# Kernel optimization log

Measured on AMD Instinct MI355X. Metric: run time of the kernel, lower is better.

Reference implementation:

```python
import jax, jax.numpy as jnp
import numpy as np

NUM_NODES = 100000
NUM_EDGES = 1600000
INPUT_DIM = 128
NUM_LAYERS = 3
EPS = 1e-12


def setup_inputs() -> dict:
    key = jax.random.key(0)
    k1, k2, k3, k4, k5 = jax.random.split(key, 5)
    emb = jax.random.normal(k1, (NUM_NODES, INPUT_DIM), dtype=jnp.float32)
    edge_index = jax.random.randint(k2, (2, NUM_EDGES), 0, NUM_NODES, dtype=jnp.int64)
    senders = jax.random.randint(k3, (16384,), 0, NUM_NODES, dtype=jnp.int64)
    receivers = jax.random.randint(k4, (16384,), 0, NUM_NODES, dtype=jnp.int64)
    mlp_dim = INPUT_DIM * (NUM_LAYERS + 1)  # concat aggregation -> 512
    W = jax.random.normal(k5, (mlp_dim, mlp_dim), dtype=jnp.float32) * 0.02
    b = jnp.zeros((mlp_dim,), dtype=jnp.float32)
    return {"emb": emb, "edge_index": edge_index, "senders": senders,
            "receivers": receivers, "W": W, "b": b}


def _l2_normalize(x):
    # matches F.normalize(x, p=2, dim=-1) with eps=1e-12
    n = jnp.linalg.norm(x, axis=-1, keepdims=True)
    return x / jnp.maximum(n, EPS)


def reference(emb, edge_index, senders, receivers, W, b):
    src, dst = edge_index[0], edge_index[1]
    # LightGCN-style symmetric degree normalization: 1/sqrt(d_src * d_dst)
    ones = jnp.ones((src.shape[0],), dtype=emb.dtype)
    deg = jax.ops.segment_sum(ones, dst, num_segments=NUM_NODES)
    deg = jnp.maximum(deg, 1.0)
    dinv = jax.lax.rsqrt(deg)
    norm = dinv[src] * dinv[dst]  # [E]

    x = emb
    z = [_l2_normalize(x)]
    for _ in range(NUM_LAYERS):
        msgs = x[src] * norm[:, None]                      # [E, D] gather + scale
        x = jax.ops.segment_sum(msgs, dst, num_segments=NUM_NODES)  # scatter-add
        z.append(_l2_normalize(x))
    x = jnp.concatenate(z, axis=-1)        # [N, D*(L+1)]
    x = x @ W.T + b                        # post_mlp
    return (x[senders], x[receivers])
```

## Files before the change

kernel.cpp:

```cpp
#include <hip/hip_runtime.h>

#define NN 100000
#define NE 1600000
#define DD 128
#define MD 512
#define SEL 16384
#define MROWS 32768
#define NBKT 196
#define TILE 4096
#define SEGCAP 16384
#define NBINA ((NE + TILE - 1) / TILE)
#define NMARK ((2 * SEL + 255) / 256)
#define NCOMP ((NN + 255) / 256)

typedef __attribute__((ext_vector_type(8))) short bf16x8;
typedef __attribute__((ext_vector_type(4))) float f32x4;

__device__ __forceinline__ unsigned short f2bf(float f) {
  unsigned u = __float_as_uint(f);
  u += 0x7fff + ((u >> 16) & 1);
  return (unsigned short)(u >> 16);
}
__device__ __forceinline__ float bflo(unsigned v) { return __uint_as_float(v << 16); }
__device__ __forceinline__ float bfhi(unsigned v) { return __uint_as_float(v & 0xffff0000u); }

__global__ __launch_bounds__(256) void k_binA_mark(const int* __restrict__ src,
                                                   const int* __restrict__ dst,
                                                   int* __restrict__ gcursor,
                                                   unsigned* __restrict__ ebuf,
                                                   const int* __restrict__ sl,
                                                   const int* __restrict__ rl,
                                                   int* __restrict__ mark) {
  if (blockIdx.x >= NBINA) {
    const int i = (blockIdx.x - NBINA) * 256 + threadIdx.x;
    if (i < SEL) mark[sl[i]] = 1;
    else if (i < 2 * SEL) mark[rl[i - SEL]] = 1;
    return;
  }
  __shared__ int hist[NBKT];
  __shared__ int base[NBKT];
  __shared__ int cnt2[NBKT];
  const int tid = threadIdx.x;
  const long e0 = (long)blockIdx.x * TILE;
  for (int i = tid; i < NBKT; i += 256) { hist[i] = 0; cnt2[i] = 0; }
  __syncthreads();
  unsigned pk[16]; int bk[16];
  #pragma unroll
  for (int k = 0; k < 16; ++k) {
    const long e = e0 + k * 256 + tid;
    bk[k] = -1;
    if (e < NE) {
      const int d = dst[e], s = src[e];
      bk[k] = d >> 9;
      pk[k] = ((unsigned)s << 9) | (unsigned)(d & 511);
      atomicAdd(&hist[bk[k]], 1);
    }
  }
  __syncthreads();
  for (int i = tid; i < NBKT; i += 256)
    base[i] = i * SEGCAP + atomicAdd(&gcursor[i], hist[i]);
  __syncthreads();
  #pragma unroll
  for (int k = 0; k < 16; ++k) {
    if (bk[k] >= 0) {
      const int lp = atomicAdd(&cnt2[bk[k]], 1);
      ebuf[base[bk[k]] + lp] = pk[k];
    }
  }
}

__global__ __launch_bounds__(256) void k_degB_compact(const unsigned* __restrict__ ebuf,
                                                      const int* __restrict__ bcnt,
                                                      int* __restrict__ deg,
                                                      float* __restrict__ dinv,
                                                      int* __restrict__ excl,
                                                      int* __restrict__ btot,
                                                      unsigned short* __restrict__ x0,
                                                      unsigned short* __restrict__ x1,
                                                      unsigned short* __restrict__ x2,
                                                      const int* __restrict__ mark,
                                                      int* __restrict__ list,
                                                      int* __restrict__ lcnt,
                                                      int* __restrict__ uidx) {
  if (blockIdx.x >= NBKT) {
    const int n = (blockIdx.x - NBKT) * 256 + threadIdx.x;
    if (n < NN && mark[n]) {
      const int p = atomicAdd(lcnt, 1);
      list[p] = n;
      uidx[n] = p;
    }
    return;
  }
  __shared__ int ld[512];
  __shared__ int ps[256];
  const int b = blockIdx.x;
  const int n0 = b << 9;
  const int nn = min(512, NN - n0);
  const int tid = threadIdx.x;
  for (int i = tid; i < 512; i += 256) ld[i] = 0;
  __syncthreads();
  const int s0 = b * SEGCAP;
  const int c = bcnt[b];
  for (int i = tid; i < c; i += 256) atomicAdd(&ld[ebuf[s0 + i] & 511], 1);
  __syncthreads();
  const int d0 = (tid * 2 < nn) ? ld[tid * 2] : 0;
  const int d1 = (tid * 2 + 1 < nn) ? ld[tid * 2 + 1] : 0;
  const int p0 = (d0 + 7) & ~7, p1 = (d1 + 7) & ~7;
  ps[tid] = p0 + p1;
  __syncthreads();
  for (int o = 1; o < 256; o <<= 1) {
    int t2 = (tid >= o) ? ps[tid - o] : 0;
    __syncthreads();
    ps[tid] += t2;
    __syncthreads();
  }
  const int exbase = ps[tid] - (p0 + p1);
  if (tid * 2 < nn) {
    deg[n0 + tid * 2] = d0;
    dinv[n0 + tid * 2] = rsqrtf(fmaxf((float)d0, 1.f));
    excl[n0 + tid * 2] = exbase;
  }
  if (tid * 2 + 1 < nn) {
    deg[n0 + tid * 2 + 1] = d1;
    dinv[n0 + tid * 2 + 1] = rsqrtf(fmaxf((float)d1, 1.f));
    excl[n0 + tid * 2 + 1] = exbase + p0;
  }
  if (tid == 255) btot[b] = ps[255];
  if (b == 0 && tid < 64) {
    ((unsigned*)(x0 + (size_t)NN * DD))[tid] = 0u;
    ((unsigned*)(x1 + (size_t)NN * DD))[tid] = 0u;
    ((unsigned*)(x2 + (size_t)NN * DD))[tid] = 0u;
  }
}

__global__ __launch_bounds__(256) void k_binB(const unsigned* __restrict__ ebuf,
                                              const int* __restrict__ bcnt,
                                              const int* __restrict__ btot,
                                              const int* __restrict__ excl,
                                              const int* __restrict__ degI,
                                              int2* __restrict__ nodeinfo,
                                              int* __restrict__ csr) {
  __shared__ int seg[SEGCAP];
  __shared__ int rs[512];
  __shared__ int cnt[512];
  __shared__ int sm[256];
  const int b = blockIdx.x;
  const int n0 = b << 9;
  const int nn = min(512, NN - n0);
  const int tid = threadIdx.x;
  int v = (tid < NBKT) ? btot[tid] : 0;
  sm[tid] = v;
  __syncthreads();
  for (int o = 1; o < 256; o <<= 1) {
    int t2 = (tid >= o) ? sm[tid - o] : 0;
    __syncthreads();
    sm[tid] += t2;
    __syncthreads();
  }
  const int seg0 = b ? sm[b - 1] : 0;
  const int seglen = btot[b];
  for (int i = tid; i < nn; i += 256) {
    const int ex = excl[n0 + i];
    rs[i] = ex;
    cnt[i] = 0;
    const int cp = (degI[n0 + i] + 7) & ~7;
    nodeinfo[n0 + i] = make_int2(seg0 + ex, cp);
  }
  for (int i = tid; i < seglen; i += 256) seg[i] = NN << 8;
  __syncthreads();
  const int s0 = b * SEGCAP;
  const int c = bcnt[b];
  for (int i = tid; i < c; i += 256) {
    const unsigned e = ebuf[s0 + i];
    const int dl = e & 511;
    const int pos = rs[dl] + atomicAdd(&cnt[dl], 1);
    seg[pos] = (int)((e >> 9) << 8);
  }
  __syncthreads();
  for (int i = tid; i < seglen; i += 256) csr[seg0 + i] = seg[i];
}

__global__ __launch_bounds__(256) void k_aggs(const int2* __restrict__ nodeinfo,
                                              const int* __restrict__ csr,
                                              const float* __restrict__ dinv,
                                              const unsigned short* __restrict__ xin,
                                              unsigned short* __restrict__ xout) {
  const int lane = threadIdx.x & 63;
  const int hi = lane >> 5, l5 = lane & 31;
  const int bid = blockIdx.x;
  const int xcd = bid & 7;
  const int h = xcd >> 2;
  const int g = (bid >> 3) * 4 + (xcd & 3);
  const int wvh = g * 4 + (threadIdx.x >> 6);
  const int stride = gridDim.x * 2;
  const char* xb = (const char*)xin;
  const unsigned lc = (unsigned)(h * 128 + l5 * 4);
  for (int p = wvh; 2 * p < NN; p += stride) {
    const int idx = 2 * p + hi;
    const bool act = idx < NN;
    const int n = act ? idx : 0;
    const int2 ni = nodeinfo[n];
    const int start = ni.x;
    const int cntp = act ? ni.y : 0;
    float ax[8], ay[8];
    #pragma unroll
    for (int u = 0; u < 8; ++u) { ax[u] = 0.f; ay[u] = 0.f; }
    for (int j = 0; j < cntp; j += 8) {
      const int4 e0 = *(const int4*)(csr + start + j);
      const int4 e1 = *(const int4*)(csr + start + j + 4);
      unsigned v[8];
      v[0] = *(const unsigned*)(xb + ((unsigned)e0.x + lc));
      v[1] = *(const unsigned*)(xb + ((unsigned)e0.y + lc));
      v[2] = *(const unsigned*)(xb + ((unsigned)e0.z + lc));
      v[3] = *(const unsigned*)(xb + ((unsigned)e0.w + lc));
      v[4] = *(const unsigned*)(xb + ((unsigned)e1.x + lc));
      v[5] = *(const unsigned*)(xb + ((unsigned)e1.y + lc));
      v[6] = *(const unsigned*)(xb + ((unsigned)e1.z + lc));
      v[7] = *(const unsigned*)(xb + ((unsigned)e1.w + lc));
      #pragma unroll
      for (int u = 0; u < 8; ++u) { ax[u] += bflo(v[u]); ay[u] += bfhi(v[u]); }
    }
    if (act) {
      const float s = dinv[n] * dinv[n];
      const float rx = (((ax[0] + ax[1]) + (ax[2] + ax[3])) + ((ax[4] + ax[5]) + (ax[6] + ax[7]))) * s;
      const float ry = (((ay[0] + ay[1]) + (ay[2] + ay[3])) + ((ay[4] + ay[5]) + (ay[6] + ay[7]))) * s;
      *(unsigned*)((char*)xout + ((unsigned)n << 8) + lc) =
          ((unsigned)f2bf(ry) << 16) | f2bf(rx);
    }
  }
}

__global__ __launch_bounds__(256) void k_agg3z(const int2* __restrict__ nodeinfo,
                                               const int* __restrict__ csr,
                                               const float* __restrict__ dinv,
                                               const unsigned short* __restrict__ x0,
                                               const unsigned short* __restrict__ x1,
                                               const unsigned short* __restrict__ x2,
                                               unsigned short* __restrict__ zbuf,
                                               const int* __restrict__ list,
                                               const int* __restrict__ lcnt) {
  const int lane = threadIdx.x & 63;
  const int wv = (blockIdx.x * blockDim.x + threadIdx.x) >> 6;
  const int nw = (gridDim.x * blockDim.x) >> 6;
  const int cl = *lcnt;
  const char* xb2 = (const char*)x2;
  const unsigned lc = (unsigned)(lane * 4);
  for (int r = wv; r < cl; r += nw) {
    const int n = list[r];
    const int2 ni = nodeinfo[n];
    const int start = ni.x;
    const int cntp = ni.y;
    float ax[8], ay[8];
    #pragma unroll
    for (int u = 0; u < 8; ++u) { ax[u] = 0.f; ay[u] = 0.f; }
    for (int j = 0; j < cntp; j += 8) {
      const int4 e0 = *(const int4*)(csr + start + j);
      const int4 e1 = *(const int4*)(csr + start + j + 4);
      unsigned v[8];
      v[0] = *(const unsigned*)(xb2 + ((unsigned)e0.x + lc));
      v[1] = *(const unsigned*)(xb2 + ((unsigned)e0.y + lc));
      v[2] = *(const unsigned*)(xb2 + ((unsigned)e0.z + lc));
      v[3] = *(const unsigned*)(xb2 + ((unsigned)e0.w + lc));
      v[4] = *(const unsigned*)(xb2 + ((unsigned)e1.x + lc));
      v[5] = *(const unsigned*)(xb2 + ((unsigned)e1.y + lc));
      v[6] = *(const unsigned*)(xb2 + ((unsigned)e1.z + lc));
      v[7] = *(const unsigned*)(xb2 + ((unsigned)e1.w + lc));
      #pragma unroll
      for (int u = 0; u < 8; ++u) { ax[u] += bflo(v[u]); ay[u] += bfhi(v[u]); }
    }
    const float s = dinv[n] * dinv[n];
    const float rx = (((ax[0] + ax[1]) + (ax[2] + ax[3])) + ((ax[4] + ax[5]) + (ax[6] + ax[7]))) * s;
    const float ry = (((ay[0] + ay[1]) + (ay[2] + ay[3])) + ((ay[4] + ay[5]) + (ay[6] + ay[7]))) * s;
    {
      float ss = fmaf(rx, rx, ry * ry);
      #pragma unroll
      for (int m = 32; m >= 1; m >>= 1) ss += __shfl_xor(ss, m);
      const float sc = 1.0f / fmaxf(sqrtf(ss), 1e-12f);
      *(unsigned*)(zbuf + (size_t)r * MD + 384 + lane * 2) =
          ((unsigned)f2bf(ry * sc) << 16) | f2bf(rx * sc);
    }
    unsigned v0 = *(const unsigned*)((const char*)x0 + ((unsigned)n << 8) + lc);
    unsigned v1 = *(const unsigned*)((const char*)x1 + ((unsigned)n << 8) + lc);
    unsigned v2 = *(const unsigned*)((const char*)x2 + ((unsigned)n << 8) + lc);
    unsigned vv[3] = {v0, v1, v2};
    #pragma unroll
    for (int q = 0; q < 3; ++q) {
      const float a = bflo(vv[q]), b = bfhi(vv[q]);
      float ss = fmaf(a, a, b * b);
      #pragma unroll
      for (int m = 32; m >= 1; m >>= 1) ss += __shfl_xor(ss, m);
      const float sc = 1.0f / fmaxf(sqrtf(ss), 1e-12f);
      *(unsigned*)(zbuf + (size_t)r * MD + q * DD + lane * 2) =
          ((unsigned)f2bf(b * sc) << 16) | f2bf(a * sc);
    }
  }
}

__global__ __launch_bounds__(256) void k_conv_emb2(const float* __restrict__ emb,
                                                   const float* __restrict__ dinv,
                                                   unsigned short* __restrict__ x0,
                                                   const float* __restrict__ W,
                                                   unsigned short* __restrict__ Wbf) {
  if (blockIdx.x >= NN / 4) {
    const int i = (blockIdx.x - NN / 4) * 256 + threadIdx.x;
    if (i < MD * MD / 4) {
      float4 v = ((const float4*)W)[i];
      ushort4 o;
      o.x = f2bf(v.x); o.y = f2bf(v.y); o.z = f2bf(v.z); o.w = f2bf(v.w);
      ((ushort4*)Wbf)[i] = o;
    }
    return;
  }
  const int lane = threadIdx.x & 63;
  const int n = blockIdx.x * 4 + (threadIdx.x >> 6);
  const float2 v = ((const float2*)(emb + (size_t)n * DD))[lane];
  const float d = dinv[n];
  *(unsigned*)(x0 + (size_t)n * DD + lane * 2) =
      ((unsigned)f2bf(v.y * d) << 16) | f2bf(v.x * d);
}

__global__ __launch_bounds__(256) void k_gemm(const unsigned short* __restrict__ zbuf,
                                              const int* __restrict__ sl,
                                              const int* __restrict__ rl,
                                              const int* __restrict__ uidx,
                                              const unsigned short* __restrict__ B,
                                              const float* __restrict__ bias,
                                              float* __restrict__ out) {
  __shared__ __align__(16) char smraw[20480];
  unsigned short (*As)[40] = (unsigned short(*)[40])smraw;
  unsigned short (*Bs)[40] = (unsigned short(*)[40])(smraw + 10240);
  float (*et)[132] = (float(*)[132])smraw;
  const int t = threadIdx.x;
  const int bid = blockIdx.x;
  const int xcd = bid & 7;
  const int j = bid >> 3;
  const int mt = xcd * 32 + (j >> 2);
  const int nt = j & 3;
  const int i0 = mt * 128, j0 = nt * 128;
  const int lane = t & 63, wid = t >> 6;
  const int wr = wid >> 1, wc = wid & 1;
  const int fr = lane & 15, kg = lane >> 4;
  const int srow = t >> 2, seg = t & 3;
  const int r0 = i0 + srow, r1 = r0 + 64;
  const int nd0 = (r0 < SEL) ? sl[r0] : rl[r0 - SEL];
  const int nd1 = (r1 < SEL) ? sl[r1] : rl[r1 - SEL];
  const unsigned short* pa0 = zbuf + (size_t)uidx[nd0] * MD + seg * 8;
  const unsigned short* pa1 = zbuf + (size_t)uidx[nd1] * MD + seg * 8;
  const unsigned short* pb0 = B + (size_t)(j0 + srow) * MD + seg * 8;
  const unsigned short* pb1 = B + (size_t)(j0 + srow + 64) * MD + seg * 8;
  f32x4 acc[4][4] = {};
  for (int k0 = 0; k0 < MD; k0 += 32) {
    *(float4*)(&As[srow][seg * 8]) = *(const float4*)(pa0 + k0);
    *(float4*)(&As[srow + 64][seg * 8]) = *(const float4*)(pa1 + k0);
    *(float4*)(&Bs[srow][seg * 8]) = *(const float4*)(pb0 + k0);
    *(float4*)(&Bs[srow + 64][seg * 8]) = *(const float4*)(pb1 + k0);
    __syncthreads();
    bf16x8 af[4], bfr[4];
    #pragma unroll
    for (int m = 0; m < 4; ++m)
      af[m] = *(const bf16x8*)(&As[wr * 64 + m * 16 + fr][kg * 8]);
    #pragma unroll
    for (int n = 0; n < 4; ++n)
      bfr[n] = *(const bf16x8*)(&Bs[wc * 64 + n * 16 + fr][kg * 8]);
    #pragma unroll
    for (int m = 0; m < 4; ++m)
      #pragma unroll
      for (int n = 0; n < 4; ++n)
        acc[m][n] = __builtin_amdgcn_mfma_f32_16x16x32_bf16(af[m], bfr[n], acc[m][n], 0, 0, 0);
    __syncthreads();
  }
  #pragma unroll
  for (int m = 0; m < 4; ++m) {
    __syncthreads();
    #pragma unroll
    for (int n = 0; n < 4; ++n)
      #pragma unroll
      for (int r = 0; r < 4; ++r)
        et[wr * 16 + kg * 4 + r][wc * 64 + n * 16 + fr] = acc[m][n][r];
    __syncthreads();
    #pragma unroll
    for (int w = 0; w < 4; ++w) {
      const int idx = w * 256 + t;
      const int lrow = idx >> 5, lc4 = idx & 31;
      const int grow = i0 + (lrow >> 4) * 64 + m * 16 + (lrow & 15);
      const int gcol = j0 + lc4 * 4;
      const float4 bv = *(const float4*)(bias + gcol);
      float4 o;
      o.x = et[lrow][lc4 * 4 + 0] + bv.x;
      o.y = et[lrow][lc4 * 4 + 1] + bv.y;
      o.z = et[lrow][lc4 * 4 + 2] + bv.z;
      o.w = et[lrow][lc4 * 4 + 3] + bv.w;
      *(float4*)(out + (size_t)grow * MD + gcol) = o;
    }
  }
}

extern "C" void kernel_launch(void* const* d_in, const int* in_sizes, int n_in,
                              void* d_out, int out_size, void* d_ws, size_t ws_size,
                              hipStream_t stream) {
  const float* emb = (const float*)d_in[0];
  const int* ei = (const int*)d_in[1];
  const int* esrc = ei;
  const int* edst = ei + NE;
  const int* send = (const int*)d_in[2];
  const int* recv = (const int*)d_in[3];
  const float* W = (const float*)d_in[4];
  const float* bias = (const float*)d_in[5];
  float* out = (float*)d_out;

  char* ws = (char*)d_ws;
  size_t off = 0;
  auto take = [&](size_t b) {
    char* p = ws + off;
    off = (off + b + 1023) & ~(size_t)1023;
    return p;
  };
  const size_t CSRN = (size_t)NE + 8 * (size_t)NN;
  int* zblk = (int*)take((size_t)(NBKT + 1 + NN) * 4);
  int* gcursor = zblk;
  int* lcnt = zblk + NBKT;
  int* mark = zblk + NBKT + 1;
  int* uidx = (int*)take((size_t)NN * 4);
  float* dinv = (float*)take((size_t)NN * 4);
  int* degI = (int*)take((size_t)NN * 4);
  int* excl = (int*)take((size_t)NN * 4);
  int2* nodeinfo = (int2*)take((size_t)NN * 8);
  int* btot = (int*)take(NBKT * 4);
  int* list = (int*)take((size_t)MROWS * 4);
  unsigned* ebuf = (unsigned*)take((size_t)NBKT * SEGCAP * 4);
  int* csr = (int*)take(CSRN * 4);
  unsigned short* x0 = (unsigned short*)take((size_t)(NN + 1) * DD * 2);
  unsigned short* x1 = (unsigned short*)take((size_t)(NN + 1) * DD * 2);
  unsigned short* x2 = (unsigned short*)take((size_t)(NN + 1) * DD * 2);
  unsigned short* zbuf = (unsigned short*)take((size_t)MROWS * MD * 2);
  unsigned short* Wbf = (unsigned short*)take((size_t)MD * MD * 2);
  (void)ws_size; (void)in_sizes; (void)n_in; (void)out_size;

  hipMemsetAsync(zblk, 0, (size_t)(NBKT + 1 + NN) * 4, stream);

  k_binA_mark<<<NBINA + NMARK, 256, 0, stream>>>(esrc, edst, gcursor, ebuf,
                                                 send, recv, mark);
  k_degB_compact<<<NBKT + NCOMP, 256, 0, stream>>>(ebuf, gcursor, degI, dinv, excl,
                                                   btot, x0, x1, x2, mark, list,
                                                   lcnt, uidx);
  k_binB<<<NBKT, 256, 0, stream>>>(ebuf, gcursor, btot, excl, degI, nodeinfo, csr);
  k_conv_emb2<<<NN / 4 + MD * MD / 4 / 256, 256, 0, stream>>>(emb, dinv, x0, W, Wbf);

  k_aggs<<<4096, 256, 0, stream>>>(nodeinfo, csr, dinv, x0, x1);
  k_aggs<<<4096, 256, 0, stream>>>(nodeinfo, csr, dinv, x1, x2);
  k_agg3z<<<2048, 256, 0, stream>>>(nodeinfo, csr, dinv, x0, x1, x2,
                                    zbuf, list, lcnt);

  k_gemm<<<(MROWS / 128) * (MD / 128), 256, 0, stream>>>(zbuf, send, recv, uidx,
                                                         Wbf, bias, out);
}
```

Before: 263.5 us.

## Fuse degree and CSR-build kernels with fixed per-bucket CSR stride; prefetch indices

```diff
diff --git a/kernel.cpp b/kernel.cpp
--- a/kernel.cpp
+++ b/kernel.cpp
@@ -9,6 +9,7 @@
 #define NBKT 196
 #define TILE 4096
 #define SEGCAP 16384
+#define CSTRIDE 12288
 #define NBINA ((NE + TILE - 1) / TILE)
 #define NMARK ((2 * SEL + 255) / 256)
 #define NCOMP ((NN + 255) / 256)
@@ -69,19 +70,18 @@
   }
 }
 
-__global__ __launch_bounds__(256) void k_degB_compact(const unsigned* __restrict__ ebuf,
-                                                      const int* __restrict__ bcnt,
-                                                      int* __restrict__ deg,
-                                                      float* __restrict__ dinv,
-                                                      int* __restrict__ excl,
-                                                      int* __restrict__ btot,
-                                                      unsigned short* __restrict__ x0,
-                                                      unsigned short* __restrict__ x1,
-                                                      unsigned short* __restrict__ x2,
-                                                      const int* __restrict__ mark,
-                                                      int* __restrict__ list,
-                                                      int* __restrict__ lcnt,
-                                                      int* __restrict__ uidx) {
+__global__ __launch_bounds__(256) void k_degbinB(const unsigned* __restrict__ ebuf,
+                                                 const int* __restrict__ bcnt,
+                                                 float* __restrict__ dinv,
+                                                 int4* __restrict__ nodeinfo,
+                                                 int* __restrict__ csr,
+                                                 unsigned short* __restrict__ x0,
+                                                 unsigned short* __restrict__ x1,
+                                                 unsigned short* __restrict__ x2,
+                                                 const int* __restrict__ mark,
+                                                 int* __restrict__ list,
+                                                 int* __restrict__ lcnt,
+                                                 int* __restrict__ uidx) {
   if (blockIdx.x >= NBKT) {
     const int n = (blockIdx.x - NBKT) * 256 + threadIdx.x;
     if (n < NN && mark[n]) {
@@ -93,6 +93,9 @@
   }
   __shared__ int ld[512];
   __shared__ int ps[256];
+  __shared__ int rs[512];
+  __shared__ int cnt[512];
+  __shared__ int seg[CSTRIDE];
   const int b = blockIdx.x;
   const int n0 = b << 9;
   const int nn = min(512, NN - n0);
@@ -115,61 +118,23 @@
     __syncthreads();
   }
   const int exbase = ps[tid] - (p0 + p1);
+  const int cb = b * CSTRIDE;
   if (tid * 2 < nn) {
-    deg[n0 + tid * 2] = d0;
-    dinv[n0 + tid * 2] = rsqrtf(fmaxf((float)d0, 1.f));
-    excl[n0 + tid * 2] = exbase;
+    const float dv = rsqrtf(fmaxf((float)d0, 1.f));
+    dinv[n0 + tid * 2] = dv;
+    rs[tid * 2] = exbase;
+    nodeinfo[n0 + tid * 2] = make_int4(cb + exbase, p0, __float_as_int(dv * dv), 0);
   }
   if (tid * 2 + 1 < nn) {
-    deg[n0 + tid * 2 + 1] = d1;
-    dinv[n0 + tid * 2 + 1] = rsqrtf(fmaxf((float)d1, 1.f));
-    excl[n0 + tid * 2 + 1] = exbase + p0;
-  }
-  if (tid == 255) btot[b] = ps[255];
-  if (b == 0 && tid < 64) {
-    ((unsigned*)(x0 + (size_t)NN * DD))[tid] = 0u;
-    ((unsigned*)(x1 + (size_t)NN * DD))[tid] = 0u;
-    ((unsigned*)(x2 + (size_t)NN * DD))[tid] = 0u;
-  }
-}
-
-__global__ __launch_bounds__(256) void k_binB(const unsigned* __restrict__ ebuf,
-                                              const int* __restrict__ bcnt,
-                                              const int* __restrict__ btot,
-                                              const int* __restrict__ excl,
-                                              const int* __restrict__ degI,
-                                              int2* __restrict__ nodeinfo,
-                                              int* __restrict__ csr) {
-  __shared__ int seg[SEGCAP];
-  __shared__ int rs[512];
-  __shared__ int cnt[512];
-  __shared__ int sm[256];
-  const int b = blockIdx.x;
-  const int n0 = b << 9;
-  const int nn = min(512, NN - n0);
-  const int tid = threadIdx.x;
-  int v = (tid < NBKT) ? btot[tid] : 0;
-  sm[tid] = v;
-  __syncthreads();
-  for (int o = 1; o < 256; o <<= 1) {
-    int t2 = (tid >= o) ? sm[tid - o] : 0;
-    __syncthreads();
-    sm[tid] += t2;
-    __syncthreads();
-  }
-  const int seg0 = b ? sm[b - 1] : 0;
-  const int seglen = btot[b];
-  for (int i = tid; i < nn; i += 256) {
-    const int ex = excl[n0 + i];
-    rs[i] = ex;
-    cnt[i] = 0;
-    const int cp = (degI[n0 + i] + 7) & ~7;
-    nodeinfo[n0 + i] = make_int2(seg0 + ex, cp);
-  }
-  for (int i = tid; i < seglen; i += 256) seg[i] = NN << 8;
-  __syncthreads();
-  const int s0 = b * SEGCAP;
-  const int c = bcnt[b];
+    const float dv = rsqrtf(fmaxf((float)d1, 1.f));
+    dinv[n0 + tid * 2 + 1] = dv;
+    rs[tid * 2 + 1] = exbase + p0;
+    nodeinfo[n0 + tid * 2 + 1] = make_int4(cb + exbase + p0, p1, __float_as_int(dv * dv), 0);
+  }
+  const int padtot = ps[255];
+  for (int i = tid; i < nn; i += 256) cnt[i] = 0;
+  for (int i = tid; i < padtot; i += 256) seg[i] = NN << 8;
+  __syncthreads();
   for (int i = tid; i < c; i += 256) {
     const unsigned e = ebuf[s0 + i];
     const int dl = e & 511;
@@ -177,12 +142,16 @@
     seg[pos] = (int)((e >> 9) << 8);
   }
   __syncthreads();
-  for (int i = tid; i < seglen; i += 256) csr[seg0 + i] = seg[i];
-}
-
-__global__ __launch_bounds__(256) void k_aggs(const int2* __restrict__ nodeinfo,
+  for (int i = tid; i < padtot; i += 256) csr[cb + i] = seg[i];
+  if (b == 0 && tid < 64) {
+    ((unsigned*)(x0 + (size_t)NN * DD))[tid] = 0u;
+    ((unsigned*)(x1 + (size_t)NN * DD))[tid] = 0u;
+    ((unsigned*)(x2 + (size_t)NN * DD))[tid] = 0u;
+  }
+}
+
+__global__ __launch_bounds__(256) void k_aggs(const int4* __restrict__ nodeinfo,
                                               const int* __restrict__ csr,
-                                              const float* __restrict__ dinv,
                                               const unsigned short* __restrict__ xin,
                                               unsigned short* __restrict__ xout) {
   const int lane = threadIdx.x & 63;
@@ -195,44 +164,55 @@
   const int stride = gridDim.x * 2;
   const char* xb = (const char*)xin;
   const unsigned lc = (unsigned)(h * 128 + l5 * 4);
-  for (int p = wvh; 2 * p < NN; p += stride) {
+  int p = wvh;
+  if (2 * p >= NN) return;
+  int4 ni = nodeinfo[min(2 * p + hi, NN - 1)];
+  for (; 2 * p < NN; p += stride) {
     const int idx = 2 * p + hi;
     const bool act = idx < NN;
-    const int n = act ? idx : 0;
-    const int2 ni = nodeinfo[n];
-    const int start = ni.x;
-    const int cntp = act ? ni.y : 0;
+    const int4 cur = ni;
+    const int pn = p + stride;
+    if (2 * pn < NN) ni = nodeinfo[min(2 * pn + hi, NN - 1)];
+    const int start = cur.x;
+    const int cntp = act ? cur.y : 0;
     float ax[8], ay[8];
     #pragma unroll
     for (int u = 0; u < 8; ++u) { ax[u] = 0.f; ay[u] = 0.f; }
+    int4 e0, e1;
+    if (cntp > 0) {
+      e0 = *(const int4*)(csr + start);
+      e1 = *(const int4*)(csr + start + 4);
+    }
     for (int j = 0; j < cntp; j += 8) {
-      const int4 e0 = *(const int4*)(csr + start + j);
-      const int4 e1 = *(const int4*)(csr + start + j + 4);
+      const int4 f0 = e0, f1 = e1;
+      if (j + 8 < cntp) {
+        e0 = *(const int4*)(csr + start + j + 8);
+        e1 = *(const int4*)(csr + start + j + 12);
+      }
       unsigned v[8];
-      v[0] = *(const unsigned*)(xb + ((unsigned)e0.x + lc));
-      v[1] = *(const unsigned*)(xb + ((unsigned)e0.y + lc));
-      v[2] = *(const unsigned*)(xb + ((unsigned)e0.z + lc));
-      v[3] = *(const unsigned*)(xb + ((unsigned)e0.w + lc));
-      v[4] = *(const unsigned*)(xb + ((unsigned)e1.x + lc));
-      v[5] = *(const unsigned*)(xb + ((unsigned)e1.y + lc));
-      v[6] = *(const unsigned*)(xb + ((unsigned)e1.z + lc));
-      v[7] = *(const unsigned*)(xb + ((unsigned)e1.w + lc));
+      v[0] = *(const unsigned*)(xb + ((unsigned)f0.x + lc));
+      v[1] = *(const unsigned*)(xb + ((unsigned)f0.y + lc));
+      v[2] = *(const unsigned*)(xb + ((unsigned)f0.z + lc));
+      v[3] = *(const unsigned*)(xb + ((unsigned)f0.w + lc));
+      v[4] = *(const unsigned*)(xb + ((unsigned)f1.x + lc));
+      v[5] = *(const unsigned*)(xb + ((unsigned)f1.y + lc));
+      v[6] = *(const unsigned*)(xb + ((unsigned)f1.z + lc));
+      v[7] = *(const unsigned*)(xb + ((unsigned)f1.w + lc));
       #pragma unroll
       for (int u = 0; u < 8; ++u) { ax[u] += bflo(v[u]); ay[u] += bfhi(v[u]); }
     }
     if (act) {
-      const float s = dinv[n] * dinv[n];
+      const float s = __int_as_float(cur.z);
       const float rx = (((ax[0] + ax[1]) + (ax[2] + ax[3])) + ((ax[4] + ax[5]) + (ax[6] + ax[7]))) * s;
       const float ry = (((ay[0] + ay[1]) + (ay[2] + ay[3])) + ((ay[4] + ay[5]) + (ay[6] + ay[7]))) * s;
-      *(unsigned*)((char*)xout + ((unsigned)n << 8) + lc) =
+      *(unsigned*)((char*)xout + ((unsigned)idx << 8) + lc) =
           ((unsigned)f2bf(ry) << 16) | f2bf(rx);
     }
   }
 }
 
-__global__ __launch_bounds__(256) void k_agg3z(const int2* __restrict__ nodeinfo,
+__global__ __launch_bounds__(256) void k_agg3z(const int4* __restrict__ nodeinfo,
                                                const int* __restrict__ csr,
-                                               const float* __restrict__ dinv,
                                                const unsigned short* __restrict__ x0,
                                                const unsigned short* __restrict__ x1,
                                                const unsigned short* __restrict__ x2,
@@ -245,30 +225,40 @@
   const int cl = *lcnt;
   const char* xb2 = (const char*)x2;
   const unsigned lc = (unsigned)(lane * 4);
-  for (int r = wv; r < cl; r += nw) {
-    const int n = list[r];
-    const int2 ni = nodeinfo[n];
+  int r = wv;
+  if (r >= cl) return;
+  int nln = list[r];
+  for (; r < cl; r += nw) {
+    const int n = nln;
+    const int rn = r + nw;
+    if (rn < cl) nln = list[rn];
+    const int4 ni = nodeinfo[n];
     const int start = ni.x;
     const int cntp = ni.y;
     float ax[8], ay[8];
     #pragma unroll
     for (int u = 0; u < 8; ++u) { ax[u] = 0.f; ay[u] = 0.f; }
+    int4 e0 = *(const int4*)(csr + start);
+    int4 e1 = *(const int4*)(csr + start + 4);
     for (int j = 0; j < cntp; j += 8) {
-      const int4 e0 = *(const int4*)(csr + start + j);
-      const int4 e1 = *(const int4*)(csr + start + j + 4);
+      const int4 f0 = e0, f1 = e1;
+      if (j + 8 < cntp) {
+        e0 = *(const int4*)(csr + start + j + 8);
+        e1 = *(const int4*)(csr + start + j + 12);
+      }
       unsigned v[8];
-      v[0] = *(const unsigned*)(xb2 + ((unsigned)e0.x + lc));
-      v[1] = *(const unsigned*)(xb2 + ((unsigned)e0.y + lc));
-      v[2] = *(const unsigned*)(xb2 + ((unsigned)e0.z + lc));
-      v[3] = *(const unsigned*)(xb2 + ((unsigned)e0.w + lc));
-      v[4] = *(const unsigned*)(xb2 + ((unsigned)e1.x + lc));
-      v[5] = *(const unsigned*)(xb2 + ((unsigned)e1.y + lc));
-      v[6] = *(const unsigned*)(xb2 + ((unsigned)e1.z + lc));
-      v[7] = *(const unsigned*)(xb2 + ((unsigned)e1.w + lc));
+      v[0] = *(const unsigned*)(xb2 + ((unsigned)f0.x + lc));
+      v[1] = *(const unsigned*)(xb2 + ((unsigned)f0.y + lc));
+      v[2] = *(const unsigned*)(xb2 + ((unsigned)f0.z + lc));
+      v[3] = *(const unsigned*)(xb2 + ((unsigned)f0.w + lc));
+      v[4] = *(const unsigned*)(xb2 + ((unsigned)f1.x + lc));
+      v[5] = *(const unsigned*)(xb2 + ((unsigned)f1.y + lc));
+      v[6] = *(const unsigned*)(xb2 + ((unsigned)f1.z + lc));
+      v[7] = *(const unsigned*)(xb2 + ((unsigned)f1.w + lc));
       #pragma unroll
       for (int u = 0; u < 8; ++u) { ax[u] += bflo(v[u]); ay[u] += bfhi(v[u]); }
     }
-    const float s = dinv[n] * dinv[n];
+    const float s = __int_as_float(ni.z);
     const float rx = (((ax[0] + ax[1]) + (ax[2] + ax[3])) + ((ax[4] + ax[5]) + (ax[6] + ax[7]))) * s;
     const float ry = (((ay[0] + ay[1]) + (ay[2] + ay[3])) + ((ay[4] + ay[5]) + (ay[6] + ay[7]))) * s;
     {
@@ -415,20 +405,16 @@
     off = (off + b + 1023) & ~(size_t)1023;
     return p;
   };
-  const size_t CSRN = (size_t)NE + 8 * (size_t)NN;
   int* zblk = (int*)take((size_t)(NBKT + 1 + NN) * 4);
   int* gcursor = zblk;
   int* lcnt = zblk + NBKT;
   int* mark = zblk + NBKT + 1;
   int* uidx = (int*)take((size_t)NN * 4);
   float* dinv = (float*)take((size_t)NN * 4);
-  int* degI = (int*)take((size_t)NN * 4);
-  int* excl = (int*)take((size_t)NN * 4);
-  int2* nodeinfo = (int2*)take((size_t)NN * 8);
-  int* btot = (int*)take(NBKT * 4);
+  int4* nodeinfo = (int4*)take((size_t)NN * 16);
   int* list = (int*)take((size_t)MROWS * 4);
   unsigned* ebuf = (unsigned*)take((size_t)NBKT * SEGCAP * 4);
-  int* csr = (int*)take(CSRN * 4);
+  int* csr = (int*)take((size_t)NBKT * CSTRIDE * 4);
   unsigned short* x0 = (unsigned short*)take((size_t)(NN + 1) * DD * 2);
   unsigned short* x1 = (unsigned short*)take((size_t)(NN + 1) * DD * 2);
   unsigned short* x2 = (unsigned short*)take((size_t)(NN + 1) * DD * 2);
@@ -440,16 +426,13 @@
 
   k_binA_mark<<<NBINA + NMARK, 256, 0, stream>>>(esrc, edst, gcursor, ebuf,
                                                  send, recv, mark);
-  k_degB_compact<<<NBKT + NCOMP, 256, 0, stream>>>(ebuf, gcursor, degI, dinv, excl,
-                                                   btot, x0, x1, x2, mark, list,
-                                                   lcnt, uidx);
-  k_binB<<<NBKT, 256, 0, stream>>>(ebuf, gcursor, btot, excl, degI, nodeinfo, csr);
+  k_degbinB<<<NBKT + NCOMP, 256, 0, stream>>>(ebuf, gcursor, dinv, nodeinfo, csr,
+                                              x0, x1, x2, mark, list, lcnt, uidx);
   k_conv_emb2<<<NN / 4 + MD * MD / 4 / 256, 256, 0, stream>>>(emb, dinv, x0, W, Wbf);
 
-  k_aggs<<<4096, 256, 0, stream>>>(nodeinfo, csr, dinv, x0, x1);
-  k_aggs<<<4096, 256, 0, stream>>>(nodeinfo, csr, dinv, x1, x2);
-  k_agg3z<<<2048, 256, 0, stream>>>(nodeinfo, csr, dinv, x0, x1, x2,
-                                    zbuf, list, lcnt);
+  k_aggs<<<4096, 256, 0, stream>>>(nodeinfo, csr, x0, x1);
+  k_aggs<<<4096, 256, 0, stream>>>(nodeinfo, csr, x1, x2);
+  k_agg3z<<<2048, 256, 0, stream>>>(nodeinfo, csr, x0, x1, x2, zbuf, list, lcnt);
 
   k_gemm<<<(MROWS / 128) * (MD / 128), 256, 0, stream>>>(zbuf, send, recv, uidx,
                                                          Wbf, bias, out);
```

New measurement: 253.5 us. 3.8% less time.
